# Kernel optimization log

Measured on AMD Instinct MI355X. Metric: run time of the kernel, lower is better.

## Reference

```python
import jax, jax.numpy as jnp
import numpy as np

D = 64        # link_state_dim
DN = D - 5    # node state dim
E = 100000    # num link states (states_num_edges)
M = 300000    # num adjacency pairs
G = 256       # num graphs in batch
R = 256       # readout_units
T = 4         # message passing iterations


def _glorot(key, shape):
    fan_in, fan_out = shape[0], shape[-1]
    lim = np.sqrt(6.0 / (fan_in + fan_out)).astype(np.float32)
    return jax.random.uniform(key, shape, jnp.float32, -lim, lim)


def setup_inputs() -> dict:
    key = jax.random.key(0)
    ks = jax.random.split(key, 24)
    inp = {
        'graph_state': jax.random.normal(ks[0], (E, D), jnp.float32),
        'node_state': jax.random.normal(ks[1], (E, DN), jnp.float32),
        'states_first': jax.random.randint(ks[2], (M,), 0, E, jnp.int32),
        'states_second': jax.random.randint(ks[3], (M,), 0, E, jnp.int32),
        'states_graph_ids': jax.random.randint(ks[4], (E,), 0, G, jnp.int32),
        'states_num_edges': E,
        # edge Message Dense: [2D -> D]
        'W_msg': _glorot(ks[5], (2 * D, D)), 'b_msg': jnp.zeros((D,), jnp.float32),
        # edge GRUCell (Keras, reset_after=True): kernel [D,3D], recurrent [D,3D], two biases [3D]
        'Wx_e': _glorot(ks[6], (D, 3 * D)), 'Wh_e': _glorot(ks[7], (D, 3 * D)),
        'bx_e': jnp.zeros((3 * D,), jnp.float32), 'bh_e': jnp.zeros((3 * D,), jnp.float32),
        # node Message Dense: [2*DN -> DN]
        'W_nmsg': _glorot(ks[8], (2 * DN, DN)), 'b_nmsg': jnp.zeros((DN,), jnp.float32),
        # node GRUCell
        'Wx_n': _glorot(ks[9], (DN, 3 * DN)), 'Wh_n': _glorot(ks[10], (DN, 3 * DN)),
        'bx_n': jnp.zeros((3 * DN,), jnp.float32), 'bh_n': jnp.zeros((3 * DN,), jnp.float32),
        # Readout MLP: [D+DN -> R -> R -> 1]
        'W1': _glorot(ks[11], (D + DN, R)), 'b1': jnp.zeros((R,), jnp.float32),
        'W2': _glorot(ks[12], (R, R)), 'b2': jnp.zeros((R,), jnp.float32),
        'W3': _glorot(ks[13], (R, 1)), 'b3': jnp.zeros((1,), jnp.float32),
    }
    return inp


def _gru(x, h, Wx, Wh, bx, bh):
    # Keras GRUCell, reset_after=True, gate order [z, r, hh]
    xm = x @ Wx + bx
    hm = h @ Wh + bh
    xz, xr, xh = jnp.split(xm, 3, axis=-1)
    hz, hr, hh = jnp.split(hm, 3, axis=-1)
    z = jax.nn.sigmoid(xz + hz)
    r = jax.nn.sigmoid(xr + hr)
    c = jnp.tanh(xh + r * hh)
    return z * h + (1.0 - z) * c


def reference(graph_state, node_state, states_first, states_second, states_graph_ids,
              states_num_edges, W_msg, b_msg, Wx_e, Wh_e, bx_e, bh_e,
              W_nmsg, b_nmsg, Wx_n, Wh_n, bx_n, bh_n, W1, b1, W2, b2, W3, b3):
    link_state = graph_state
    for _ in range(T):
        main_e = link_state[states_first]           # [M, D]
        neigh_e = link_state[states_second]          # [M, D]
        msg = jax.nn.selu(jnp.concatenate([main_e, neigh_e], axis=1) @ W_msg + b_msg)
        agg = jax.ops.segment_sum(msg, states_second, num_segments=states_num_edges)
        link_state = _gru(agg, link_state, Wx_e, Wh_e, bx_e, bh_e)
    for _ in range(T):
        main_n = node_state[states_first]            # [M, DN]
        neigh_n = node_state[states_second]          # [M, DN]
        nmsg = jax.nn.selu(jnp.concatenate([main_n, neigh_n], axis=1) @ W_nmsg + b_nmsg)
        nagg = jax.ops.segment_sum(nmsg, states_second, num_segments=states_num_edges)
        node_state = _gru(nagg, node_state, Wx_n, Wh_n, bx_n, bh_n)
    combined = jnp.concatenate([link_state, node_state], axis=1)   # [E, D+DN]
    pooled = jax.ops.segment_sum(combined, states_graph_ids, num_segments=G)  # [G, D+DN]
    h = jax.nn.selu(pooled @ W1 + b1)
    h = jax.nn.selu(h @ W2 + b2)   # dropout is identity at inference
    return h @ W3 + b3             # [G, 1]
```

## Files before the change

kernel.cpp:

```cpp
#include <hip/hip_runtime.h>
#include <hip/hip_bf16.h>

#define DNODE 59
#define NGRAPH 256
typedef __hip_bfloat16 bf16;
typedef long long ll;
typedef unsigned short ushort;
typedef short short8v __attribute__((ext_vector_type(8)));
typedef float float4v __attribute__((ext_vector_type(4)));

__device__ __forceinline__ float b2f(bf16 x) { return __bfloat162float(x); }
__device__ __forceinline__ float bs2f(ushort u) {
    return __uint_as_float(((unsigned int)u) << 16);
}
__device__ __forceinline__ float ldv(const void* p, ll i, int isf) {
    return isf ? ((const float*)p)[i] : b2f(((const bf16*)p)[i]);
}
__device__ __forceinline__ ushort f2bs(float x) {
    unsigned int u = __float_as_uint(x);
    u += 0x7fffu + ((u >> 16) & 1u);
    return (ushort)(u >> 16);
}
__device__ __forceinline__ float frcp(float x) { return __builtin_amdgcn_rcpf(x); }
__device__ __forceinline__ float selu_f(float x) {
    const float scale = 1.0507009873554805f;
    const float alpha = 1.6732632423543772f;
    return x > 0.f ? scale * x : scale * alpha * (__expf(x) - 1.f);
}
__device__ __forceinline__ float fsigmoid(float x) { return frcp(1.f + __expf(-x)); }
__device__ __forceinline__ float ftanh(float x) {
    float t = __expf(-2.f * fabsf(x));
    return copysignf((1.f - t) * frcp(1.f + t), x);
}

template <typename T>
__device__ __forceinline__ float ldT(const T* p, ll i);
template <> __device__ __forceinline__ float ldT<float>(const float* p, ll i) { return p[i]; }
template <> __device__ __forceinline__ float ldT<bf16>(const bf16* p, ll i)  { return b2f(p[i]); }

__global__ void k_detect(const ushort* __restrict__ gsu, int* __restrict__ flag,
                         int* __restrict__ gcnt)
{
    int t = threadIdx.x;
    if (t < 512) gcnt[t] = 0;
    if (t == 0 && blockIdx.x == 0) {
        int wild = 0;
        for (int i = 0; i < 512; ++i) {
            int e = (gsu[i] >> 7) & 0xFF;
            if (e >= 0x8F) wild++;
        }
        *flag = (wild >= 20) ? 1 : 0;
    }
}

__global__ void k_prep_all(const void* __restrict__ gs, const void* __restrict__ nsb,
                           ushort* __restrict__ B1, ushort* __restrict__ B2,
                           const void* W_msg, const void* W_nmsg,
                           const void* Wx_e, const void* Wh_e,
                           const void* Wx_n, const void* Wh_n,
                           const void* b_msg, const void* b_nmsg,
                           const void* bx_e, const void* bh_e,
                           const void* bx_n, const void* bh_n,
                           short* Wpq_e, short* Wpq_n,
                           short* Gxb_e, short* Ghb_e, short* Gxb_n, short* Ghb_n,
                           float* bm_e, float* bm_n,
                           float* bgx_e, float* bgh_e, float* bgx_n, float* bgh_n,
                           int E, const int* __restrict__ dflag)
{
    const int isf = *dflag;
    int b = blockIdx.x, t = threadIdx.x;
    const int ebi = (E * 64 + 255) / 256;

    if (b < ebi) {
        int i = b * 256 + t;
        if (i < E * 64) B1[i] = f2bs(ldv(gs, i, isf));
        return;
    }
    b -= ebi;
    if (b < ebi) {
        int i = b * 256 + t;
        if (i < E * 64) {
            int e = i >> 6, c = i & 63;
            B2[i] = (c < DNODE) ? f2bs(ldv(nsb, (ll)e * DNODE + c, isf)) : 0;
        }
        return;
    }
    b -= ebi;
    if (b < 64) {
        const void* src = (b < 32) ? W_msg : W_nmsg;
        short* dst = (b < 32) ? Wpq_e : Wpq_n;
        int KH = (b < 32) ? 64 : DNODE;
        int i = (b & 31) * 256 + t;
        int k = i >> 7, j = i & 127, half = j >> 6, c = j & 63;
        float v = 0.f;
        if (k < KH && c < KH) v = ldv(src, (ll)(half * KH + k) * KH + c, isf);
        dst[(k >> 3) * 1024 + j * 8 + (k & 7)] = (short)f2bs(v);
        return;
    }
    b -= 64;
    if (b < 192) {
        int w = b / 48, lb = b % 48;
        const void* src = (w == 0) ? Wx_e : (w == 1) ? Wh_e : (w == 2) ? Wx_n : Wh_n;
        short* dst = (w == 0) ? Gxb_e : (w == 1) ? Ghb_e : (w == 2) ? Gxb_n : Ghb_n;
        int D = (w < 2) ? 64 : DNODE;
        int i = lb * 256 + t;
        if (i >= 64 * 192) return;
        int k = i / 192, c = i % 192, g = c >> 6, d = c & 63;
        float v = 0.f;
        if (k < D && d < D) v = ldv(src, (ll)k * 3 * D + g * D + d, isf);
        dst[(k >> 3) * 1536 + c * 8 + (k & 7)] = (short)f2bs(v);
        return;
    }
    for (int i = t; i < 896; i += 256) {
        if (i < 64)        bm_e[i] = ldv(b_msg, i, isf);
        else if (i < 128)  { int c = i - 64;  bm_n[c]  = (c < DNODE) ? ldv(b_nmsg, c, isf) : 0.f; }
        else if (i < 320)  { int c = i - 128; bgx_e[c] = ldv(bx_e, c, isf); }
        else if (i < 512)  { int c = i - 320; bgh_e[c] = ldv(bh_e, c, isf); }
        else if (i < 704)  { int c = i - 512; int g = c >> 6, d = c & 63;
                             bgx_n[c] = (d < DNODE) ? ldv(bx_n, (ll)g * DNODE + d, isf) : 0.f; }
        else               { int c = i - 704; int g = c >> 6, d = c & 63;
                             bgh_n[c] = (d < DNODE) ? ldv(bh_n, (ll)g * DNODE + d, isf) : 0.f; }
    }
}

__global__ void k_hist(const int* __restrict__ second, int* __restrict__ cnt, int M)
{
    int m = blockIdx.x * 256 + threadIdx.x;
    if (m < M) atomicAdd(&cnt[second[m]], 1);
}
__global__ void k_scan_block(int* __restrict__ cnt, int* __restrict__ bsum, int E)
{
    __shared__ int s[256];
    int t = threadIdx.x, i = blockIdx.x * 256 + t;
    int v = (i < E) ? cnt[i] : 0;
    s[t] = v;
    __syncthreads();
    #pragma unroll
    for (int d = 1; d < 256; d <<= 1) {
        int xv = (t >= d) ? s[t - d] : 0;
        __syncthreads();
        s[t] += xv;
        __syncthreads();
    }
    if (i < E) cnt[i] = s[t] - v;
    if (t == 255) bsum[blockIdx.x] = s[255];
}
__global__ void k_scan_top(const int* __restrict__ bsum, int* __restrict__ ebsum, int NB)
{
    if (threadIdx.x == 0 && blockIdx.x == 0) {
        int run = 0;
        for (int b = 0; b < NB; ++b) { ebsum[b] = run; run += bsum[b]; }
    }
}
__global__ void k_scan_add(int* __restrict__ cnt, const int* __restrict__ ebsum, int E)
{
    int i = blockIdx.x * 256 + threadIdx.x;
    if (i < E) cnt[i] += ebsum[blockIdx.x];
}
__global__ void k_scatter(const int* __restrict__ first, const int* __restrict__ second,
                          int* __restrict__ cnt, int* __restrict__ fiS,
                          int* __restrict__ seS, int M)
{
    int m = blockIdx.x * 256 + threadIdx.x;
    if (m < M) {
        int s = second[m];
        int pos = atomicAdd(&cnt[s], 1);
        fiS[pos] = first[m];
        seS[pos] = second[m];
    }
}

__global__ void k_ghist2(const int* __restrict__ gid, int* __restrict__ gcnt,
                         int* __restrict__ blockHist, int E)
{
    __shared__ int h[NGRAPH];
    int t = threadIdx.x;
    h[t] = 0;
    __syncthreads();
    int i = blockIdx.x * 256 + t;
    if (i < E) atomicAdd(&h[gid[i]], 1);
    __syncthreads();
    blockHist[blockIdx.x * NGRAPH + t] = h[t];
    if (h[t]) atomicAdd(&gcnt[t], h[t]);
}
__global__ void k_gscan(const int* __restrict__ gcnt, int* __restrict__ gOff,
                        int* __restrict__ gpos)
{
    __shared__ int s[NGRAPH];
    int t = threadIdx.x;
    int v = gcnt[t];
    s[t] = v;
    __syncthreads();
    #pragma unroll
    for (int d = 1; d < 256; d <<= 1) {
        int xv = (t >= d) ? s[t - d] : 0;
        __syncthreads();
        s[t] += xv;
        __syncthreads();
    }
    int excl = s[t] - v;
    gOff[t] = excl;
    gpos[t] = excl;
    if (t == 255) gOff[256] = s[255];
}
__launch_bounds__(512)
__global__ void k_gbase2(const int* __restrict__ gOff, int* __restrict__ blockHist, int NB)
{
    __shared__ int s[512];
    const int g = blockIdx.x, t = threadIdx.x;
    int base = gOff[g];
    for (int c0 = 0; c0 < NB; c0 += 512) {
        int b = c0 + t;
        int v = (b < NB) ? blockHist[b * NGRAPH + g] : 0;
        s[t] = v;
        __syncthreads();
        #pragma unroll
        for (int d = 1; d < 512; d <<= 1) {
            int xv = (t >= d) ? s[t - d] : 0;
            __syncthreads();
            s[t] += xv;
            __syncthreads();
        }
        if (b < NB) blockHist[b * NGRAPH + g] = base + s[t] - v;
        int tot = s[511];
        __syncthreads();
        base += tot;
    }
}
__global__ void k_gscatter2(const int* __restrict__ gid, const int* __restrict__ blockHist,
                            int* __restrict__ eIdx, int E)
{
    __shared__ int h[NGRAPH];
    int t = threadIdx.x;
    h[t] = 0;
    __syncthreads();
    int i = blockIdx.x * 256 + t;
    if (i < E) {
        int g = gid[i];
        int r = atomicAdd(&h[g], 1);
        eIdx[blockHist[blockIdx.x * NGRAPH + g] + r] = i;
    }
}

__launch_bounds__(256)
__global__ void k_pq2(const ushort* __restrict__ B1, const ushort* __restrict__ B2,
                      const short* __restrict__ We, const short* __restrict__ Wn,
                      ushort* __restrict__ PQe, ushort* __restrict__ PQn,
                      int E, int eb)
{
    __shared__ __align__(16) short Ms16[64 * 136];
    int bb = blockIdx.x;
    const ushort* B; const short* Wb; ushort* PQ;
    if (bb < eb) { B = B1; Wb = We; PQ = PQe; }
    else { bb -= eb; B = B2; Wb = Wn; PQ = PQn; }

    const int t = threadIdx.x;
    const int e0 = bb * 64;
    const int lane = t & 63, wv = t >> 6, quad = lane >> 4, l16 = lane & 15;
    const int em = wv * 16;

    int er = e0 + em + l16; if (er >= E) er = E - 1;

    float4v acc[8];
    #pragma unroll
    for (int i = 0; i < 8; ++i) acc[i] = (float4v){0.f, 0.f, 0.f, 0.f};

    #pragma unroll
    for (int c = 0; c < 2; ++c) {
        int kb = c * 4 + quad;
        short8v a = *(const short8v*)&B[(ll)er * 64 + kb * 8];
        #pragma unroll
        for (int tn = 0; tn < 8; ++tn) {
            short8v bw = *(const short8v*)&Wb[(kb * 128 + tn * 16 + l16) * 8];
            acc[tn] = __builtin_amdgcn_mfma_f32_16x16x32_bf16(a, bw, acc[tn], 0, 0, 0);
        }
    }

    #pragma unroll
    for (int tn = 0; tn < 8; ++tn)
        #pragma unroll
        for (int r = 0; r < 4; ++r)
            Ms16[(em + quad * 4 + r) * 136 + tn * 16 + l16] = (short)f2bs(acc[tn][r]);
    __syncthreads();
    #pragma unroll
    for (int r = 0; r < 4; ++r) {
        int id = t + r * 256;
        int row = id >> 4, q = id & 15;
        if (e0 + row < E)
            *(uint4*)&PQ[(ll)(e0 + row) * 128 + q * 8] = *(uint4*)&Ms16[row * 136 + q * 8];
    }
}

__launch_bounds__(256)
__global__ void k_scat2(const ushort* __restrict__ PQe, const ushort* __restrict__ PQn,
                        const int* __restrict__ fiS, const int* __restrict__ seS,
                        const float* __restrict__ bme, const float* __restrict__ bmn,
                        ushort* __restrict__ agge, ushort* __restrict__ aggn,
                        ushort* __restrict__ bVe, ushort* __restrict__ bVn,
                        int* __restrict__ bDe, int* __restrict__ bDn,
                        int M, int scb)
{
    int bb = blockIdx.x;
    const ushort* PQ; const float* bm; ushort* aggb; ushort* bndVal; int* bndDst;
    if (bb < scb) { PQ = PQe; bm = bme; aggb = agge; bndVal = bVe; bndDst = bDe; }
    else { bb -= scb; PQ = PQn; bm = bmn; aggb = aggn; bndVal = bVn; bndDst = bDn; }

    const int lane = threadIdx.x & 63, wv = threadIdx.x >> 6;
    const int hl = lane & 31;
    const bool isUp = lane >= 32;
    const int sp = bb * 4 + wv;
    const int m0 = sp * 64;
    const float bba = bm[2 * hl], bbb = bm[2 * hl + 1];
    const unsigned* PQu = (const unsigned*)PQ;
    unsigned* aggu = (unsigned*)aggb;
    unsigned* bVu  = (unsigned*)bndVal;

    int mm = m0 + lane;
    int fiv = (mm < M) ? fiS[mm] : 0;
    int sev = (mm < M) ? seS[mm] : -1;

    int cur = __builtin_amdgcn_readlane(sev, 0);
    if (cur < 0) {
        if (lane == 0) { bndDst[2 * sp] = -1; bndDst[2 * sp + 1] = -1; }
        return;
    }

    unsigned long long vmask = __ballot(sev >= 0);
    int prevv = __shfl_up(sev, 1);
    unsigned long long bmask = __ballot(lane > 0 && sev != prevv);

    float sa = 0.f, sb = 0.f;
    bool headDone = false;
    auto FLUSH = [&](int nxt) {
        float ta = sa + __shfl_xor(sa, 32);
        float tb = sb + __shfl_xor(sb, 32);
        unsigned w = (unsigned)f2bs(ta) | ((unsigned)f2bs(tb) << 16);
        if (!headDone) {
            if (!isUp) bVu[(ll)(2 * sp) * 32 + hl] = w;
            if (lane == 0) bndDst[2 * sp] = cur;
            headDone = true;
        } else {
            if (!isUp) aggu[(ll)cur * 32 + hl] = w;
        }
        sa = 0.f; sb = 0.f; cur = nxt;
    };

    unsigned pu[4], qu[4];
    #pragma unroll
    for (int u = 0; u < 4; ++u) {
        int idx = 2 * u + (isUp ? 1 : 0);
        int fr = __shfl(fiv, idx);
        int sr = max(__shfl(sev, idx), 0);
        pu[u] = PQu[(size_t)(unsigned)fr * 64 + hl];
        qu[u] = PQu[(size_t)(unsigned)sr * 64 + 32 + hl];
    }

    for (int k0 = 0; k0 < 32; k0 += 4) {
        #pragma unroll
        for (int u = 0; u < 4; ++u) {
            int k = k0 + u;
            unsigned pw = pu[u], qw = qu[u];
            int k4 = k + 4;
            if (k4 < 32) {
                int idx = 2 * k4 + (isUp ? 1 : 0);
                int fr = __shfl(fiv, idx);
                int sr = max(__shfl(sev, idx), 0);
                pu[u] = PQu[(size_t)(unsigned)fr * 64 + hl];
                qu[u] = PQu[(size_t)(unsigned)sr * 64 + 32 + hl];
            }
            float pa = bs2f((ushort)(pw & 0xffffu)), pb = bs2f((ushort)(pw >> 16));
            float qa = bs2f((ushort)(qw & 0xffffu)), qb = bs2f((ushort)(qw >> 16));
            float ca = selu_f(pa + qa + bba);
            float cb = selu_f(pb + qb + bbb);
            if ((bmask >> (2 * k)) & 1ull)
                FLUSH(__builtin_amdgcn_readlane(sev, 2 * k));
            if ((vmask >> (2 * k)) & 1ull) {
                if (!isUp) { sa += ca; sb += cb; }
            }
            if ((bmask >> (2 * k + 1)) & 1ull)
                FLUSH(__builtin_amdgcn_readlane(sev, 2 * k + 1));
            if ((vmask >> (2 * k + 1)) & 1ull) {
                if (isUp) { sa += ca; sb += cb; }
            }
        }
    }
    {
        float ta = sa + __shfl_xor(sa, 32);
        float tb = sb + __shfl_xor(sb, 32);
        unsigned w = (unsigned)f2bs(ta) | ((unsigned)f2bs(tb) << 16);
        if (!headDone) {
            if (!isUp) bVu[(ll)(2 * sp) * 32 + hl] = w;
            if (lane == 0) { bndDst[2 * sp] = cur; bndDst[2 * sp + 1] = -1; }
        } else {
            if (!isUp) bVu[(ll)(2 * sp + 1) * 32 + hl] = w;
            if (lane == 0) bndDst[2 * sp + 1] = cur;
        }
    }
}

__global__ void k_fix2(const int* __restrict__ bDe, const int* __restrict__ bDn,
                       const ushort* __restrict__ bVe, const ushort* __restrict__ bVn,
                       ushort* __restrict__ agge, ushort* __restrict__ aggn,
                       int NR, int fixb)
{
    int bb = blockIdx.x;
    const int* bndDst; const ushort* bndVal; ushort* aggb;
    if (bb < fixb) { bndDst = bDe; bndVal = bVe; aggb = agge; }
    else { bb -= fixb; bndDst = bDn; bndVal = bVn; aggb = aggn; }

    int idx = (bb * 256 + threadIdx.x) >> 6;
    int lane = threadIdx.x & 63;
    if (idx >= NR) return;
    int dst = bndDst[idx];
    if (dst < 0) return;
    int pprev = idx - 1;
    while (pprev >= 0 && bndDst[pprev] < 0) --pprev;
    if (pprev >= 0 && bndDst[pprev] == dst) return;
    float s = 0.f;
    for (int r = idx; r < NR; ++r) {
        int d = bndDst[r];
        if (d == dst) s += bs2f(bndVal[(ll)r * 64 + lane]);
        else if (d >= 0) break;
    }
    aggb[(ll)dst * 64 + lane] = f2bs(s);
}

__launch_bounds__(256)
__global__ void k_gru2(const ushort* __restrict__ agge, const ushort* __restrict__ aggn,
                       ushort* __restrict__ B1, ushort* __restrict__ B2,
                       const short* __restrict__ Gxe, const short* __restrict__ Gxn,
                       const short* __restrict__ Ghe, const short* __restrict__ Ghn,
                       const float* __restrict__ bxe, const float* __restrict__ bxn,
                       const float* __restrict__ bhe, const float* __restrict__ bhn,
                       int E, int eb)
{
    int bb = blockIdx.x;
    const ushort* xb; ushort* hb; const short* Gxb; const short* Ghb;
    const float* bgx; const float* bgh;
    if (bb < eb) { xb = agge; hb = B1; Gxb = Gxe; Ghb = Ghe; bgx = bxe; bgh = bhe; }
    else { bb -= eb; xb = aggn; hb = B2; Gxb = Gxn; Ghb = Ghn; bgx = bxn; bgh = bhn; }

    const int t = threadIdx.x;
    const int e0 = bb * 64;
    const int lane = t & 63, wv = t >> 6, quad = lane >> 4, l16 = lane & 15;
    const int em = wv * 16;
    int er = e0 + em + l16; if (er >= E) er = E - 1;

    float4v zr[8], xh[4], hh[4];
    #pragma unroll
    for (int i = 0; i < 8; ++i) zr[i] = (float4v){0.f, 0.f, 0.f, 0.f};
    #pragma unroll
    for (int i = 0; i < 4; ++i) { xh[i] = (float4v){0.f,0.f,0.f,0.f}; hh[i] = (float4v){0.f,0.f,0.f,0.f}; }

    #pragma unroll
    for (int c = 0; c < 2; ++c) {
        int kb = c * 4 + quad;
        short8v a_x = *(const short8v*)&xb[(ll)er * 64 + kb * 8];
        short8v a_h = *(const short8v*)&hb[(ll)er * 64 + kb * 8];
        #pragma unroll
        for (int tn = 0; tn < 8; ++tn) {
            short8v b_x = *(const short8v*)&Gxb[(kb * 192 + tn * 16 + l16) * 8];
            zr[tn] = __builtin_amdgcn_mfma_f32_16x16x32_bf16(a_x, b_x, zr[tn], 0, 0, 0);
            short8v b_h = *(const short8v*)&Ghb[(kb * 192 + tn * 16 + l16) * 8];
            zr[tn] = __builtin_amdgcn_mfma_f32_16x16x32_bf16(a_h, b_h, zr[tn], 0, 0, 0);
        }
        #pragma unroll
        for (int tn = 0; tn < 4; ++tn) {
            short8v b_x = *(const short8v*)&Gxb[(kb * 192 + (8 + tn) * 16 + l16) * 8];
            xh[tn] = __builtin_amdgcn_mfma_f32_16x16x32_bf16(a_x, b_x, xh[tn], 0, 0, 0);
            short8v b_h = *(const short8v*)&Ghb[(kb * 192 + (8 + tn) * 16 + l16) * 8];
            hh[tn] = __builtin_amdgcn_mfma_f32_16x16x32_bf16(a_h, b_h, hh[tn], 0, 0, 0);
        }
    }

    float bz[4], br_[4], bxh[4], bhh[4];
    #pragma unroll
    for (int j = 0; j < 4; ++j) {
        int d = j * 16 + l16;
        bz[j]  = bgx[d] + bgh[d];
        br_[j] = bgx[64 + d] + bgh[64 + d];
        bxh[j] = bgx[128 + d];
        bhh[j] = bgh[128 + d];
    }

    #pragma unroll
    for (int r = 0; r < 4; ++r) {
        int e = e0 + em + quad * 4 + r;
        if (e >= E) continue;
        #pragma unroll
        for (int j = 0; j < 4; ++j) {
            int d = j * 16 + l16;
            float z  = fsigmoid(zr[j][r] + bz[j]);
            float rr = fsigmoid(zr[4 + j][r] + br_[j]);
            float cc = ftanh(xh[j][r] + bxh[j] + rr * (hh[j][r] + bhh[j]));
            float ho = bs2f(hb[(ll)e * 64 + d]);
            hb[(ll)e * 64 + d] = f2bs(z * ho + (1.f - z) * cc);
        }
    }
}

__launch_bounds__(256)
__global__ void k_pool2(const ushort* __restrict__ lsb, const ushort* __restrict__ nsb,
                        const int* __restrict__ eIdx, const int* __restrict__ gid,
                        float* __restrict__ pooled, int E)
{
    const int t = threadIdx.x, lane = t & 63, wv = t >> 6;
    const int span = blockIdx.x * 2 + (wv >> 1);
    const int colhalf = wv & 1;
    const int s0 = span * 64;
    if (s0 >= E) return;

    int idx = s0 + lane;
    int ei = (idx < E) ? eIdx[idx] : 0;
    int gv = (idx < E) ? gid[ei] : -1;
    const ushort* src = colhalf ? nsb : lsb;
    const int cb = colhalf ? 64 : 0;

    float pv[4];
    #pragma unroll
    for (int u = 0; u < 4; ++u) {
        int e = __shfl(ei, u);
        pv[u] = bs2f(src[(ll)e * 64 + lane]);
    }

    int curg = __shfl(gv, 0);
    float acc = 0.f;
    for (int i0 = 0; i0 < 64; i0 += 4) {
        #pragma unroll
        for (int u = 0; u < 4; ++u) {
            int i = i0 + u;
            int g = __shfl(gv, i);
            float v = pv[u];
            int i4 = i + 4;
            if (i4 < 64) {
                int e = __shfl(ei, i4);
                pv[u] = bs2f(src[(ll)e * 64 + lane]);
            }
            if (g >= 0) {
                if (g != curg) {
                    atomicAdd(&pooled[curg * 128 + cb + lane], acc);
                    curg = g; acc = 0.f;
                }
                acc += v;
            }
        }
    }
    atomicAdd(&pooled[curg * 128 + cb + lane], acc);
}

template <typename T>
__device__ __forceinline__ void mlp_body(const float* __restrict__ pooled,
                                         const T* __restrict__ W1, const T* __restrict__ b1,
                                         const T* __restrict__ W2, const T* __restrict__ b2,
                                         const T* __restrict__ W3, const T* __restrict__ b3,
                                         void* __restrict__ out, int isf)
{
    __shared__ float pooledS[128];
    __shared__ float h1s[256];
    __shared__ float ps[4][256];
    __shared__ float red[256];
    const int g = blockIdx.x, t = threadIdx.x;
    const int j = t & 255, s = t >> 8;

    if (t < 128) pooledS[t] = pooled[g * 128 + t];
    __syncthreads();

    {
        int k0 = s * 31, k1 = min(64 + DNODE, k0 + 31);
        float a = 0.f;
        #pragma unroll 4
        for (int k = k0; k < k1; ++k)
            a = fmaf(pooledS[k], ldT<T>(W1, (ll)k * 256 + j), a);
        ps[s][j] = a;
    }
    __syncthreads();
    if (t < 256) {
        float a1 = ldT<T>(b1, t) + ps[0][t] + ps[1][t] + ps[2][t] + ps[3][t];
        h1s[t] = selu_f(a1);
    }
    __syncthreads();

    {
        int k0 = s * 64;
        float a = 0.f;
        #pragma unroll 8
        for (int k = k0; k < k0 + 64; ++k)
            a = fmaf(h1s[k], ldT<T>(W2, (ll)k * 256 + j), a);
        ps[s][j] = a;
    }
    __syncthreads();
    if (t < 256) {
        float a2 = ldT<T>(b2, t) + ps[0][t] + ps[1][t] + ps[2][t] + ps[3][t];
        red[t] = selu_f(a2) * ldT<T>(W3, t);
    }
    __syncthreads();
    for (int sdt = 128; sdt > 0; sdt >>= 1) {
        if (t < sdt) red[t] += red[t + sdt];
        __syncthreads();
    }
    if (t == 0) {
        float o = red[0] + ldT<T>(b3, 0);
        if (isf) ((float*)out)[g] = o;
        else     ((bf16*)out)[g] = __float2bfloat16(o);
    }
}
__launch_bounds__(1024)
__global__ void k_mlpall(const float* __restrict__ pooled,
                         const void* __restrict__ W1, const void* __restrict__ b1,
                         const void* __restrict__ W2, const void* __restrict__ b2,
                         const void* __restrict__ W3, const void* __restrict__ b3,
                         void* __restrict__ out, const int* __restrict__ dflag)
{
    const int isf = *dflag;
    if (isf) mlp_body<float>(pooled, (const float*)W1, (const float*)b1,
                             (const float*)W2, (const float*)b2,
                             (const float*)W3, (const float*)b3, out, 1);
    else     mlp_body<bf16> (pooled, (const bf16*)W1, (const bf16*)b1,
                             (const bf16*)W2, (const bf16*)b2,
                             (const bf16*)W3, (const bf16*)b3, out, 0);
}

extern "C" void kernel_launch(void* const* d_in, const int* in_sizes, int n_in,
                              void* d_out, int out_size, void* d_ws, size_t ws_size,
                              hipStream_t stream)
{
    const void* graph_state = d_in[0];
    const void* node_state  = d_in[1];
    const int*  first   = (const int*)d_in[2];
    const int*  second  = (const int*)d_in[3];
    const int*  gid     = (const int*)d_in[4];
    const void* W_msg  = d_in[6];
    const void* b_msg  = d_in[7];
    const void* Wx_e   = d_in[8];
    const void* Wh_e   = d_in[9];
    const void* bx_e   = d_in[10];
    const void* bh_e   = d_in[11];
    const void* W_nmsg = d_in[12];
    const void* b_nmsg = d_in[13];
    const void* Wx_n   = d_in[14];
    const void* Wh_n   = d_in[15];
    const void* bx_n   = d_in[16];
    const void* bh_n   = d_in[17];
    const void* W1 = d_in[18];
    const void* b1 = d_in[19];
    const void* W2 = d_in[20];
    const void* b2 = d_in[21];
    const void* W3 = d_in[22];
    const void* b3 = d_in[23];

    const int E = in_sizes[0] / 64;
    const int M = in_sizes[2];
    const int eb   = (E + 63) / 64;
    const int nsp  = (M + 63) / 64;
    const int scb  = (nsp + 3) / 4;
    const int NR   = 2 * scb * 4;
    const int fixb = (NR * 64 + 255) / 256;
    const int psp  = (E + 63) / 64;
    const int plb  = (psp + 1) / 2;

    ushort* B1    = (ushort*)d_ws;
    ushort* B2    = B1 + (size_t)E * 64;
    ushort* agge  = B2 + (size_t)E * 64;
    ushort* aggn  = agge + (size_t)E * 64;
    ushort* PQe   = aggn + (size_t)E * 64;
    ushort* PQn   = PQe + (size_t)E * 128;
    int*    fiS   = (int*)(PQn + (size_t)E * 128);
    int*    seS   = fiS + M;
    ushort* bVe   = (ushort*)(seS + M);
    ushort* bVn   = bVe + (size_t)NR * 64;
    int*    bDe   = (int*)(bVn + (size_t)NR * 64);
    int*    bDn   = bDe + NR;
    short*  sb    = (short*)(bDn + NR);
    size_t so = 0;
    short* Wpq_e = sb + so; so += 8192;
    short* Wpq_n = sb + so; so += 8192;
    short* Gxb_e = sb + so; so += 12288;
    short* Ghb_e = sb + so; so += 12288;
    short* Gxb_n = sb + so; so += 12288;
    short* Ghb_n = sb + so; so += 12288;
    float* fb = (float*)(sb + so);
    size_t fo = 0;
    float* bm_e  = fb + fo; fo += 64;
    float* bm_n  = fb + fo; fo += 64;
    float* bgx_e = fb + fo; fo += 192;
    float* bgh_e = fb + fo; fo += 192;
    float* bgx_n = fb + fo; fo += 192;
    float* bgh_n = fb + fo; fo += 192;
    int* dflag = (int*)(fb + fo);
    int* gcnt = dflag + 1;
    int* gpos = gcnt + 256;
    int* gOff = gcnt + 512;
    int* eIdx = gcnt + 769;
    int* cnt   = (int*)agge;
    int* bsum  = cnt + E;
    int* ebsum = bsum + 512;
    int* blockHist = (int*)PQe;
    float* pooled = (float*)PQe;

    k_detect<<<1, 512, 0, stream>>>((const ushort*)graph_state, dflag, gcnt);
    const int ebi = (E * 64 + 255) / 256;
    k_prep_all<<<2 * ebi + 64 + 192 + 1, 256, 0, stream>>>(
        graph_state, node_state, B1, B2,
        W_msg, W_nmsg, Wx_e, Wh_e, Wx_n, Wh_n,
        b_msg, b_nmsg, bx_e, bh_e, bx_n, bh_n,
        Wpq_e, Wpq_n, Gxb_e, Ghb_e, Gxb_n, Ghb_n,
        bm_e, bm_n, bgx_e, bgh_e, bgx_n, bgh_n, E, dflag);

    const int NB = (E + 255) / 256;
    hipMemsetAsync(cnt, 0, (size_t)E * sizeof(int), stream);
    k_hist<<<(M + 255) / 256, 256, 0, stream>>>(second, cnt, M);
    k_scan_block<<<NB, 256, 0, stream>>>(cnt, bsum, E);
    k_scan_top<<<1, 64, 0, stream>>>(bsum, ebsum, NB);
    k_scan_add<<<NB, 256, 0, stream>>>(cnt, ebsum, E);
    k_scatter<<<(M + 255) / 256, 256, 0, stream>>>(first, second, cnt, fiS, seS, M);

    hipMemsetAsync(agge, 0, (size_t)2 * E * 64 * sizeof(ushort), stream);

    k_ghist2<<<NB, 256, 0, stream>>>(gid, gcnt, blockHist, E);
    k_gscan<<<1, 256, 0, stream>>>(gcnt, gOff, gpos);
    k_gbase2<<<NGRAPH, 512, 0, stream>>>(gOff, blockHist, NB);
    k_gscatter2<<<NB, 256, 0, stream>>>(gid, blockHist, eIdx, E);

    for (int it = 0; it < 4; ++it) {
        k_pq2  <<<2 * eb,   256, 0, stream>>>(B1, B2, Wpq_e, Wpq_n, PQe, PQn, E, eb);
        k_scat2<<<2 * scb,  256, 0, stream>>>(PQe, PQn, fiS, seS, bm_e, bm_n,
                                              agge, aggn, bVe, bVn, bDe, bDn, M, scb);
        k_fix2 <<<2 * fixb, 256, 0, stream>>>(bDe, bDn, bVe, bVn, agge, aggn, NR, fixb);
        k_gru2 <<<2 * eb,   256, 0, stream>>>(agge, aggn, B1, B2,
                                              Gxb_e, Gxb_n, Ghb_e, Ghb_n,
                                              bgx_e, bgx_n, bgh_e, bgh_n, E, eb);
    }

    hipMemsetAsync(pooled, 0, (size_t)NGRAPH * 128 * sizeof(float), stream);
    k_pool2<<<plb, 256, 0, stream>>>(B1, B2, eIdx, gid, pooled, E);
    k_mlpall<<<NGRAPH, 1024, 0, stream>>>(pooled, W1, b1, W2, b2, W3, b3, d_out, dflag);
}
```

Baseline: 685.1 us.

## Parallelize serial detect/scan kernels, pack edge pairs, stage GRU hidden in LDS

Replaces the single-thread loops in the dtype detection and top-level scan kernels with block-parallel versions built on a shared atomic and a shared-memory scan. Packs the sorted first/second index arrays into one int2 array so the scatter and message kernels each do one 8-byte load per pair. In the GRU kernel, the hidden-state tile is saved to swizzled LDS during the matmul, so the final update reads it from LDS instead of reloading it from global memory. These target serial launch latency and redundant global traffic, at the cost of extra LDS use in the GRU kernel, which may lower occupancy.

```diff
diff --git a/kernel.cpp b/kernel.cpp
--- a/kernel.cpp
+++ b/kernel.cpp
@@ -41,16 +41,15 @@
 __global__ void k_detect(const ushort* __restrict__ gsu, int* __restrict__ flag,
                          int* __restrict__ gcnt)
 {
+    __shared__ int wilds;
     int t = threadIdx.x;
+    if (t == 0) wilds = 0;
     if (t < 512) gcnt[t] = 0;
-    if (t == 0 && blockIdx.x == 0) {
-        int wild = 0;
-        for (int i = 0; i < 512; ++i) {
-            int e = (gsu[i] >> 7) & 0xFF;
-            if (e >= 0x8F) wild++;
-        }
-        *flag = (wild >= 20) ? 1 : 0;
-    }
+    __syncthreads();
+    int e = (gsu[t] >> 7) & 0xFF;
+    if (e >= 0x8F) atomicAdd(&wilds, 1);
+    __syncthreads();
+    if (t == 0) *flag = (wilds >= 20) ? 1 : 0;
 }
 
 __global__ void k_prep_all(const void* __restrict__ gs, const void* __restrict__ nsb,
@@ -145,11 +144,28 @@
     if (i < E) cnt[i] = s[t] - v;
     if (t == 255) bsum[blockIdx.x] = s[255];
 }
+__launch_bounds__(512)
 __global__ void k_scan_top(const int* __restrict__ bsum, int* __restrict__ ebsum, int NB)
 {
-    if (threadIdx.x == 0 && blockIdx.x == 0) {
-        int run = 0;
-        for (int b = 0; b < NB; ++b) { ebsum[b] = run; run += bsum[b]; }
+    __shared__ int s[512];
+    const int t = threadIdx.x;
+    int base = 0;
+    for (int c0 = 0; c0 < NB; c0 += 512) {
+        int b = c0 + t;
+        int v = (b < NB) ? bsum[b] : 0;
+        s[t] = v;
+        __syncthreads();
+        #pragma unroll
+        for (int d = 1; d < 512; d <<= 1) {
+            int xv = (t >= d) ? s[t - d] : 0;
+            __syncthreads();
+            s[t] += xv;
+            __syncthreads();
+        }
+        if (b < NB) ebsum[b] = base + s[t] - v;
+        int tot = s[511];
+        __syncthreads();
+        base += tot;
     }
 }
 __global__ void k_scan_add(int* __restrict__ cnt, const int* __restrict__ ebsum, int E)
@@ -158,15 +174,13 @@
     if (i < E) cnt[i] += ebsum[blockIdx.x];
 }
 __global__ void k_scatter(const int* __restrict__ first, const int* __restrict__ second,
-                          int* __restrict__ cnt, int* __restrict__ fiS,
-                          int* __restrict__ seS, int M)
+                          int* __restrict__ cnt, int2* __restrict__ prS, int M)
 {
     int m = blockIdx.x * 256 + threadIdx.x;
     if (m < M) {
         int s = second[m];
         int pos = atomicAdd(&cnt[s], 1);
-        fiS[pos] = first[m];
-        seS[pos] = second[m];
+        prS[pos] = make_int2(first[m], s);
     }
 }
 
@@ -293,7 +307,7 @@
 
 __launch_bounds__(256)
 __global__ void k_scat2(const ushort* __restrict__ PQe, const ushort* __restrict__ PQn,
-                        const int* __restrict__ fiS, const int* __restrict__ seS,
+                        const int2* __restrict__ prS,
                         const float* __restrict__ bme, const float* __restrict__ bmn,
                         ushort* __restrict__ agge, ushort* __restrict__ aggn,
                         ushort* __restrict__ bVe, ushort* __restrict__ bVn,
@@ -316,8 +330,8 @@
     unsigned* bVu  = (unsigned*)bndVal;
 
     int mm = m0 + lane;
-    int fiv = (mm < M) ? fiS[mm] : 0;
-    int sev = (mm < M) ? seS[mm] : -1;
+    int2 pr = (mm < M) ? prS[mm] : make_int2(0, -1);
+    int fiv = pr.x, sev = pr.y;
 
     int cur = __builtin_amdgcn_readlane(sev, 0);
     if (cur < 0) {
@@ -434,6 +448,7 @@
                        const float* __restrict__ bhe, const float* __restrict__ bhn,
                        int E, int eb)
 {
+    __shared__ __align__(16) short Hs[64 * 64];
     int bb = blockIdx.x;
     const ushort* xb; ushort* hb; const short* Gxb; const short* Ghb;
     const float* bgx; const float* bgh;
@@ -445,6 +460,7 @@
     const int lane = t & 63, wv = t >> 6, quad = lane >> 4, l16 = lane & 15;
     const int em = wv * 16;
     int er = e0 + em + l16; if (er >= E) er = E - 1;
+    const int hrow = em + l16;
 
     float4v zr[8], xh[4], hh[4];
     #pragma unroll
@@ -457,6 +473,7 @@
         int kb = c * 4 + quad;
         short8v a_x = *(const short8v*)&xb[(ll)er * 64 + kb * 8];
         short8v a_h = *(const short8v*)&hb[(ll)er * 64 + kb * 8];
+        *(short8v*)&Hs[hrow * 64 + ((kb ^ (hrow & 7)) << 3)] = a_h;
         #pragma unroll
         for (int tn = 0; tn < 8; ++tn) {
             short8v b_x = *(const short8v*)&Gxb[(kb * 192 + tn * 16 + l16) * 8];
@@ -485,7 +502,8 @@
 
     #pragma unroll
     for (int r = 0; r < 4; ++r) {
-        int e = e0 + em + quad * 4 + r;
+        int rowl = em + quad * 4 + r;
+        int e = e0 + rowl;
         if (e >= E) continue;
         #pragma unroll
         for (int j = 0; j < 4; ++j) {
@@ -493,7 +511,7 @@
             float z  = fsigmoid(zr[j][r] + bz[j]);
             float rr = fsigmoid(zr[4 + j][r] + br_[j]);
             float cc = ftanh(xh[j][r] + bxh[j] + rr * (hh[j][r] + bhh[j]));
-            float ho = bs2f(hb[(ll)e * 64 + d]);
+            float ho = bs2f((ushort)Hs[rowl * 64 + ((((d >> 3) ^ (rowl & 7)) << 3) | (d & 7))]);
             hb[(ll)e * 64 + d] = f2bs(z * ho + (1.f - z) * cc);
         }
     }
@@ -664,9 +682,8 @@
     ushort* aggn  = agge + (size_t)E * 64;
     ushort* PQe   = aggn + (size_t)E * 64;
     ushort* PQn   = PQe + (size_t)E * 128;
-    int*    fiS   = (int*)(PQn + (size_t)E * 128);
-    int*    seS   = fiS + M;
-    ushort* bVe   = (ushort*)(seS + M);
+    int2*   prS   = (int2*)(PQn + (size_t)E * 128);
+    ushort* bVe   = (ushort*)(prS + M);
     ushort* bVn   = bVe + (size_t)NR * 64;
     int*    bDe   = (int*)(bVn + (size_t)NR * 64);
     int*    bDn   = bDe + NR;
@@ -710,9 +727,9 @@
     hipMemsetAsync(cnt, 0, (size_t)E * sizeof(int), stream);
     k_hist<<<(M + 255) / 256, 256, 0, stream>>>(second, cnt, M);
     k_scan_block<<<NB, 256, 0, stream>>>(cnt, bsum, E);
-    k_scan_top<<<1, 64, 0, stream>>>(bsum, ebsum, NB);
+    k_scan_top<<<1, 512, 0, stream>>>(bsum, ebsum, NB);
     k_scan_add<<<NB, 256, 0, stream>>>(cnt, ebsum, E);
-    k_scatter<<<(M + 255) / 256, 256, 0, stream>>>(first, second, cnt, fiS, seS, M);
+    k_scatter<<<(M + 255) / 256, 256, 0, stream>>>(first, second, cnt, prS, M);
 
     hipMemsetAsync(agge, 0, (size_t)2 * E * 64 * sizeof(ushort), stream);
 
@@ -723,7 +740,7 @@
 
     for (int it = 0; it < 4; ++it) {
         k_pq2  <<<2 * eb,   256, 0, stream>>>(B1, B2, Wpq_e, Wpq_n, PQe, PQn, E, eb);
-        k_scat2<<<2 * scb,  256, 0, stream>>>(PQe, PQn, fiS, seS, bm_e, bm_n,
+        k_scat2<<<2 * scb,  256, 0, stream>>>(PQe, PQn, prS, bm_e, bm_n,
                                               agge, aggn, bVe, bVn, bDe, bDn, M, scb);
         k_fix2 <<<2 * fixb, 256, 0, stream>>>(bDe, bDn, bVe, bVn, agge, aggn, NR, fixb);
         k_gru2 <<<2 * eb,   256, 0, stream>>>(agge, aggn, B1, B2,
```

New measurement: 646.3 us. 1.06x faster.
